# Performance work log

Measured on AMD Instinct MI355X. Metric: run time of the kernel, lower is better.

## Reference

```python
import jax, jax.numpy as jnp
import numpy as np

ATT_RANGE = 10
R_FACTOR = 2
NHEAD = 8

def softsign(x):
    return x / (1.0 + jnp.abs(x))

def layer_norm(x, g, b, eps=1e-5):
    mu = jnp.mean(x, axis=-1, keepdims=True)
    var = jnp.var(x, axis=-1, keepdims=True)
    return (x - mu) / jnp.sqrt(var + eps) * g + b

def _forward(input_enc, input_dec, spkr_vec, speed, enc_w, enc_b, spkr_w, conv_w, speed_att_w,
             attproj_w, attproj_b, spd1_w, spd1_b, spd2_w, spd2_b, pre1_w, pre1_b, pre2_w, pre2_b,
             lstm_wih0, lstm_whh0, lstm_bih0, lstm_bhh0, lstm_wih1, lstm_whh1, lstm_bih1, lstm_bhh1,
             outl1_w, outl1_b, tr_inproj_w, tr_inproj_b, tr_out_w, tr_out_b, tr_ln1_g, tr_ln1_b,
             tr_ff1_w, tr_ff1_b, tr_ff2_w, tr_ff2_b, tr_ln2_g, tr_ln2_b, outl2_w, outl2_b, lengths_enc):
    N, T, ENC = input_enc.shape
    # first-step attention state: one-hot at t=0 (null_state branch)
    aw0 = jnp.zeros((N, T), input_enc.dtype).at[:, 0].set(1.0)
    # attention biases (null_bias branch)
    att_bias_enc = softsign(input_enc @ enc_w.T + enc_b)          # (N,T,ATT)
    att_bias_spkr = softsign(spkr_vec @ spkr_w.T)                  # (N,1,ATT)
    in_att_speed = (speed[:, None] @ speed_att_w.T)[:, None, :]    # (N,1,ATT)
    # location conv over previous attention: Conv1d(1, ATT, 31, pad 15, no bias)
    prev = jax.lax.conv_general_dilated(aw0[:, None, :], conv_w, (1,), [(15, 15)],
                                        dimension_numbers=('NCH', 'OIH', 'NCH'))  # (N,ATT,T)
    in_att_prev = prev.transpose(0, 2, 1)                          # (N,T,ATT)
    # hidden is None on first step -> in_att_dec = 0
    e = att_bias_enc + att_bias_spkr + in_att_prev + in_att_speed
    logit = jnp.tanh(e) @ attproj_w.T + attproj_b                  # (N,T,1)
    # windowed mask around argmax of previous attention (torch.no_grad)
    m = jnp.argmax(aw0, axis=1)                                    # (N,)
    t = jnp.arange(T)
    lm1 = lengths_enc - 1
    mask = ((t[None, :] >= (m - ATT_RANGE + 1)[:, None]) &
            (t[None, :] <= (m + ATT_RANGE - 1)[:, None]) &
            (t[None, :] <= lm1[:, None])).astype(logit.dtype)[..., None]
    w = jnp.exp(logit - jnp.max(logit, axis=1, keepdims=True)) * jax.lax.stop_gradient(mask)
    w = w / jnp.maximum(jnp.sum(jnp.abs(w), axis=1, keepdims=True), 1e-12)  # F.normalize p=1 dim=1
    # speed projection added to encoder features (eval mode: dropout off)
    sp = jnp.tanh(jax.nn.relu(speed[:, None] @ spd1_w.T + spd1_b) @ spd2_w.T + spd2_b)  # (N,ENC)
    enc2 = input_enc + sp[:, None, :]
    context = jnp.einsum('nt,ntc->nc', w[..., 0], enc2)[:, None, :]  # (N,1,ENC)
    # prenet on cat(input_dec, spkr)
    pin = jnp.concatenate([input_dec, spkr_vec[:, 0, :]], axis=-1)
    pre = jax.nn.relu(jax.nn.relu(pin @ pre1_w.T + pre1_b) @ pre2_w.T + pre2_b)[:, None, :]
    in_lstm = jnp.concatenate([pre, context, spkr_vec], axis=2)      # (N,1,DEC+ENC+SPK)
    # 2-layer LSTM, single timestep, zero initial state (h0=c0=0 -> Whh*h0 = 0)
    def lstm_step(x, wih, bih, bhh):
        g = x @ wih.T + bih + bhh
        i, f, gg, o = jnp.split(g, 4, axis=-1)
        c = jax.nn.sigmoid(i) * jnp.tanh(gg)
        return jax.nn.sigmoid(o) * jnp.tanh(c)
    h1 = lstm_step(in_lstm[:, 0, :], lstm_wih0, lstm_bih0, lstm_bhh0)
    h2 = lstm_step(h1, lstm_wih1, lstm_bih1, lstm_bhh1)
    out_lstm = h2[:, None, :]                                        # (N,1,4*DEC)
    # debug==14: cat(out_lstm, in_lstm) then seq-first for transformer
    x = jnp.concatenate([out_lstm, in_lstm], axis=2).transpose(1, 0, 2)  # (1,N,3136)
    x = x @ outl1_w.T + outl1_b                                      # (1,N,DEC)
    D = x.shape[-1]
    dh = D // NHEAD
    for l in range(tr_inproj_w.shape[0]):
        qkv = x @ tr_inproj_w[l].T + tr_inproj_b[l]
        q, k, v = jnp.split(qkv, 3, axis=-1)
        S, Nn, _ = q.shape
        qh = q.reshape(S, Nn, NHEAD, dh)
        kh = k.reshape(S, Nn, NHEAD, dh)
        vh = v.reshape(S, Nn, NHEAD, dh)
        a = jnp.einsum('snhd,tnhd->nhst', qh, kh) / jnp.sqrt(jnp.asarray(dh, x.dtype))
        a = jax.nn.softmax(a, axis=-1)
        att = jnp.einsum('nhst,tnhd->snhd', a, vh).reshape(S, Nn, D)
        att = att @ tr_out_w[l].T + tr_out_b[l]
        x = layer_norm(x + att, tr_ln1_g[l], tr_ln1_b[l])
        ff = jax.nn.relu(x @ tr_ff1_w[l].T + tr_ff1_b[l]) @ tr_ff2_w[l].T + tr_ff2_b[l]
        x = layer_norm(x + ff, tr_ln2_g[l], tr_ln2_b[l])
    out = (x @ outl2_w.T + outl2_b).transpose(1, 0, 2).reshape(N, R_FACTOR, -1)  # (N,2,80)
    return out, context

def setup_inputs():
    key = jax.random.key(0)
    ks = iter(jax.random.split(key, 64))
    def nrm(shape, s=0.05):
        return jax.random.normal(next(ks), shape, jnp.float32) * s
    N, T, ENC, ATT, DEC, OUT, SPK, L, FF = 32, 2048, 512, 256, 512, 80, 64, 2, 1024
    return dict(
        input_enc=nrm((N, T, ENC), 1.0),
        input_dec=nrm((N, OUT), 1.0),
        spkr_vec=nrm((N, 1, SPK), 1.0),
        speed=jax.random.uniform(next(ks), (N,), jnp.float32, 0.5, 1.5),
        lengths_enc=jnp.full((N,), T, dtype=jnp.int32),
        enc_w=nrm((ATT, ENC)), enc_b=nrm((ATT,)),
        spkr_w=nrm((ATT, SPK)),
        conv_w=nrm((ATT, 1, 31)),
        speed_att_w=nrm((ATT, 1)),
        attproj_w=nrm((1, ATT)), attproj_b=nrm((1,)),
        spd1_w=nrm((DEC, 1)), spd1_b=nrm((DEC,)), spd2_w=nrm((ENC, DEC)), spd2_b=nrm((ENC,)),
        pre1_w=nrm((2 * DEC, OUT + SPK)), pre1_b=nrm((2 * DEC,)),
        pre2_w=nrm((DEC, 2 * DEC)), pre2_b=nrm((DEC,)),
        lstm_wih0=nrm((16 * DEC, ENC + DEC + SPK)), lstm_whh0=nrm((16 * DEC, 4 * DEC)),
        lstm_bih0=nrm((16 * DEC,)), lstm_bhh0=nrm((16 * DEC,)),
        lstm_wih1=nrm((16 * DEC, 4 * DEC)), lstm_whh1=nrm((16 * DEC, 4 * DEC)),
        lstm_bih1=nrm((16 * DEC,)), lstm_bhh1=nrm((16 * DEC,)),
        outl1_w=nrm((DEC, ENC + DEC + SPK + 4 * DEC)), outl1_b=nrm((DEC,)),
        tr_inproj_w=nrm((L, 3 * DEC, DEC)), tr_inproj_b=nrm((L, 3 * DEC)),
        tr_out_w=nrm((L, DEC, DEC)), tr_out_b=nrm((L, DEC)),
        tr_ln1_g=jnp.ones((L, DEC)), tr_ln1_b=jnp.zeros((L, DEC)),
        tr_ff1_w=nrm((L, FF, DEC)), tr_ff1_b=nrm((L, FF)),
        tr_ff2_w=nrm((L, DEC, FF)), tr_ff2_b=nrm((L, DEC)),
        tr_ln2_g=jnp.ones((L, DEC)), tr_ln2_b=jnp.zeros((L, DEC)),
        outl2_w=nrm((R_FACTOR * OUT, DEC)), outl2_b=nrm((R_FACTOR * OUT,)),
    )

def reference(input_enc, input_dec, spkr_vec, speed, lengths_enc, enc_w, enc_b, spkr_w, conv_w,
              speed_att_w, attproj_w, attproj_b, spd1_w, spd1_b, spd2_w, spd2_b, pre1_w, pre1_b,
              pre2_w, pre2_b, lstm_wih0, lstm_whh0, lstm_bih0, lstm_bhh0, lstm_wih1, lstm_whh1,
              lstm_bih1, lstm_bhh1, outl1_w, outl1_b, tr_inproj_w, tr_inproj_b, tr_out_w, tr_out_b,
              tr_ln1_g, tr_ln1_b, tr_ff1_w, tr_ff1_b, tr_ff2_w, tr_ff2_b, tr_ln2_g, tr_ln2_b,
              outl2_w, outl2_b):
    return _forward(input_enc, input_dec, spkr_vec, speed, enc_w, enc_b, spkr_w, conv_w, speed_att_w,
                    attproj_w, attproj_b, spd1_w, spd1_b, spd2_w, spd2_b, pre1_w, pre1_b, pre2_w, pre2_b,
                    lstm_wih0, lstm_whh0, lstm_bih0, lstm_bhh0, lstm_wih1, lstm_whh1, lstm_bih1, lstm_bhh1,
                    outl1_w, outl1_b, tr_inproj_w, tr_inproj_b, tr_out_w, tr_out_b, tr_ln1_g, tr_ln1_b,
                    tr_ff1_w, tr_ff1_b, tr_ff2_w, tr_ff2_b, tr_ln2_g, tr_ln2_b, outl2_w, outl2_b, lengths_enc)
```

## Files before the change

### kernel.cpp

```cpp
#include <hip/hip_runtime.h>

typedef unsigned short u16;
typedef unsigned int u32;

__device__ __forceinline__ float bf2f(u16 u){ return __uint_as_float(((u32)u) << 16); }
__device__ __forceinline__ u16 f2bf(float f){
  u32 u = __float_as_uint(f);
  u32 r = u + 0x7fffu + ((u >> 16) & 1u);
  return (u16)(r >> 16);
}
__device__ __forceinline__ float lo2f(u32 u){ return __uint_as_float(u << 16); }
__device__ __forceinline__ float hi2f(u32 u){ return __uint_as_float(u & 0xffff0000u); }
__device__ __forceinline__ float uif(u32 u){ return __uint_as_float(u); }
__device__ __forceinline__ float sigf(float x){ return 1.0f / (1.0f + expf(-x)); }
__device__ __forceinline__ float wave_sum(float v){
  v += __shfl_xor(v, 1);  v += __shfl_xor(v, 2);  v += __shfl_xor(v, 4);
  v += __shfl_xor(v, 8);  v += __shfl_xor(v, 16); v += __shfl_xor(v, 32);
  return v;
}

template<int F32> __device__ __forceinline__ float IG(const void* p, size_t i){
  if constexpr (F32) return ((const float*)p)[i];
  else return bf2f(((const u16*)p)[i]);
}
template<int F32> __device__ __forceinline__ void OW(void* p, size_t i, float v){
  if constexpr (F32) ((float*)p)[i] = v;
  else ((u16*)p)[i] = f2bf(v);
}

__global__ void k_detect(const void* speed, int* flag)
{
  if (threadIdx.x == 0 && blockIdx.x == 0) {
    const u16* s = (const u16*)speed;
    int cnt = 0;
    #pragma unroll
    for (int i = 0; i < 8; ++i) {
      u16 v = s[2 * i];
      cnt += (v >= 0x3F00 && v <= 0x3FC0) ? 1 : 0;
    }
    flag[0] = (cnt >= 6) ? 0 : 1;
  }
}

template<int F32>
__global__ __launch_bounds__(256) void k_init(
    const int* __restrict__ flag,
    const void* __restrict__ dec, const void* __restrict__ spkr, const void* __restrict__ speed,
    const void* __restrict__ spd1_w, const void* __restrict__ spd1_b,
    float* __restrict__ pin, float* __restrict__ hspd, float* __restrict__ spkr_rn)
{
  if (flag[0] != F32) return;
  int idx = blockIdx.x * 256 + threadIdx.x;
  if (idx < 144 * 32) {
    int k = idx >> 5, n = idx & 31;
    float v = (k < 80) ? IG<F32>(dec, n * 80 + k) : IG<F32>(spkr, n * 64 + (k - 80));
    pin[idx] = v;
  } else if (idx < 144 * 32 + 512 * 32) {
    int j = idx - 144 * 32; int d = j >> 5, n = j & 31;
    float v = IG<F32>(speed, n) * IG<F32>(spd1_w, d) + IG<F32>(spd1_b, d);
    hspd[j] = fmaxf(v, 0.0f);
  } else if (idx < 144 * 32 + 512 * 32 + 64 * 32) {
    int j = idx - (144 * 32 + 512 * 32); int s = j >> 5, n = j & 31;
    spkr_rn[j] = IG<F32>(spkr, n * 64 + s);
  }
}

__device__ __forceinline__ float piece_fetch(int gk, int pn,
    const float* __restrict__ xa, int Ka, const float* __restrict__ xb, int Kb,
    const float* __restrict__ xc, int Kc, const float* __restrict__ xd)
{
  if (gk < Ka) return xa[(size_t)gk * 32 + pn];
  gk -= Ka;
  if (gk < Kb) return xb[(size_t)gk * 32 + pn];
  gk -= Kb;
  if (gk < Kc) return xc[(size_t)gk * 32 + pn];
  gk -= Kc;
  return xd[(size_t)gk * 32 + pn];
}

template<int F32>
__global__ __launch_bounds__(256) void k_gemv32(
    const int* __restrict__ flag,
    const float* __restrict__ xa, int Ka,
    const float* __restrict__ xb, int Kb,
    const float* __restrict__ xc, int Kc,
    const float* __restrict__ xd,
    const void* __restrict__ W,
    const void* __restrict__ bias1,
    const void* __restrict__ bias2,
    float* __restrict__ out,
    int K, int rowmap, int act)
{
  if (flag[0] != F32) return;
  __shared__ u32 xbuf[256][33];
  const int KCHE = F32 ? 256 : 512;
  int tid = threadIdx.x;
  int n = tid & 31;
  int rl = tid >> 5;
  int r = blockIdx.x * 8 + rl;
  int wr = r;
  if (rowmap && r >= 2048) wr = r + 2048;
  float acc = 0.0f;

  for (int k0 = 0; k0 < K; k0 += KCHE) {
    int kc = K - k0; if (kc > KCHE) kc = KCHE;
    if constexpr (F32) {
      for (int p = tid; p < kc * 32; p += 256) {
        int pn = p & 31, kk = p >> 5;
        xbuf[kk][pn] = __float_as_uint(piece_fetch(k0 + kk, pn, xa, Ka, xb, Kb, xc, Kc, xd));
      }
    } else {
      int pairs = kc >> 1;
      for (int p = tid; p < pairs * 32; p += 256) {
        int pn = p & 31, kk2 = p >> 5;
        int gk = k0 + 2 * kk2;
        float v0 = piece_fetch(gk,     pn, xa, Ka, xb, Kb, xc, Kc, xd);
        float v1 = piece_fetch(gk + 1, pn, xa, Ka, xb, Kb, xc, Kc, xd);
        xbuf[kk2][pn] = ((u32)f2bf(v1) << 16) | (u32)f2bf(v0);
      }
    }
    __syncthreads();
    if constexpr (F32) {
      const float4* wq = reinterpret_cast<const float4*>((const float*)W + (size_t)wr * (size_t)K + k0);
      for (int kk = 0; kk < kc; kk += 8) {
        float4 w0 = wq[(kk >> 2)];
        float4 w1 = wq[(kk >> 2) + 1];
        acc = fmaf(uif(xbuf[kk + 0][n]), w0.x, acc);
        acc = fmaf(uif(xbuf[kk + 1][n]), w0.y, acc);
        acc = fmaf(uif(xbuf[kk + 2][n]), w0.z, acc);
        acc = fmaf(uif(xbuf[kk + 3][n]), w0.w, acc);
        acc = fmaf(uif(xbuf[kk + 4][n]), w1.x, acc);
        acc = fmaf(uif(xbuf[kk + 5][n]), w1.y, acc);
        acc = fmaf(uif(xbuf[kk + 6][n]), w1.z, acc);
        acc = fmaf(uif(xbuf[kk + 7][n]), w1.w, acc);
      }
    } else {
      int pairs = kc >> 1;
      const uint4* wq = reinterpret_cast<const uint4*>((const u16*)W + (size_t)wr * (size_t)K + k0);
      for (int kk2 = 0; kk2 < pairs; kk2 += 4) {
        uint4 wv = wq[kk2 >> 2];
        u32 xw;
        xw = xbuf[kk2 + 0][n]; acc = fmaf(lo2f(xw), lo2f(wv.x), acc); acc = fmaf(hi2f(xw), hi2f(wv.x), acc);
        xw = xbuf[kk2 + 1][n]; acc = fmaf(lo2f(xw), lo2f(wv.y), acc); acc = fmaf(hi2f(xw), hi2f(wv.y), acc);
        xw = xbuf[kk2 + 2][n]; acc = fmaf(lo2f(xw), lo2f(wv.z), acc); acc = fmaf(hi2f(xw), hi2f(wv.z), acc);
        xw = xbuf[kk2 + 3][n]; acc = fmaf(lo2f(xw), lo2f(wv.w), acc); acc = fmaf(hi2f(xw), hi2f(wv.w), acc);
      }
    }
    __syncthreads();
  }
  if (bias1) acc += IG<F32>(bias1, wr);
  if (bias2) acc += IG<F32>(bias2, wr);
  if (act == 1) acc = fmaxf(acc, 0.0f);
  else if (act == 2) acc = tanhf(acc);
  out[(size_t)r * 32 + n] = acc;
}

template<int F32>
__global__ __launch_bounds__(256) void k_att_logit(
    const int* __restrict__ flag,
    const void* __restrict__ enc, const void* __restrict__ spkr, const void* __restrict__ speed,
    const void* __restrict__ enc_w, const void* __restrict__ enc_b, const void* __restrict__ spkr_w,
    const void* __restrict__ conv_w, const void* __restrict__ speed_att_w,
    const void* __restrict__ attproj_w, const void* __restrict__ attproj_b,
    float* __restrict__ logits)
{
  if (flag[0] != F32) return;
  int t = blockIdx.x;
  int n = blockIdx.y;
  int tid = threadIdx.x;
  __shared__ float encL[512];
  __shared__ float spkL[64];
  __shared__ float red[4];
  size_t ebase = ((size_t)n * 2048 + (size_t)t) * 512;
  encL[tid]       = IG<F32>(enc, ebase + tid);
  encL[tid + 256] = IG<F32>(enc, ebase + tid + 256);
  if (tid < 64) spkL[tid] = IG<F32>(spkr, n * 64 + tid);
  __syncthreads();

  int a = tid;
  float ss = 0.0f, d = 0.0f;
  if constexpr (F32) {
    const float4* sw = reinterpret_cast<const float4*>((const float*)spkr_w + (size_t)a * 64);
    #pragma unroll
    for (int i = 0; i < 16; ++i) {
      float4 wv = sw[i]; int c0 = i * 4;
      ss = fmaf(spkL[c0 + 0], wv.x, ss); ss = fmaf(spkL[c0 + 1], wv.y, ss);
      ss = fmaf(spkL[c0 + 2], wv.z, ss); ss = fmaf(spkL[c0 + 3], wv.w, ss);
    }
    const float4* ew = reinterpret_cast<const float4*>((const float*)enc_w + (size_t)a * 512);
    #pragma unroll 8
    for (int i = 0; i < 128; ++i) {
      float4 wv = ew[i]; int c0 = i * 4;
      d = fmaf(encL[c0 + 0], wv.x, d); d = fmaf(encL[c0 + 1], wv.y, d);
      d = fmaf(encL[c0 + 2], wv.z, d); d = fmaf(encL[c0 + 3], wv.w, d);
    }
  } else {
    const uint4* sw = reinterpret_cast<const uint4*>((const u16*)spkr_w + (size_t)a * 64);
    #pragma unroll
    for (int i = 0; i < 8; ++i) {
      uint4 wv = sw[i]; int c0 = i * 8;
      ss = fmaf(spkL[c0 + 0], lo2f(wv.x), ss); ss = fmaf(spkL[c0 + 1], hi2f(wv.x), ss);
      ss = fmaf(spkL[c0 + 2], lo2f(wv.y), ss); ss = fmaf(spkL[c0 + 3], hi2f(wv.y), ss);
      ss = fmaf(spkL[c0 + 4], lo2f(wv.z), ss); ss = fmaf(spkL[c0 + 5], hi2f(wv.z), ss);
      ss = fmaf(spkL[c0 + 6], lo2f(wv.w), ss); ss = fmaf(spkL[c0 + 7], hi2f(wv.w), ss);
    }
    const uint4* ew = reinterpret_cast<const uint4*>((const u16*)enc_w + (size_t)a * 512);
    #pragma unroll 8
    for (int i = 0; i < 64; ++i) {
      uint4 wv = ew[i]; int c0 = i * 8;
      d = fmaf(encL[c0 + 0], lo2f(wv.x), d); d = fmaf(encL[c0 + 1], hi2f(wv.x), d);
      d = fmaf(encL[c0 + 2], lo2f(wv.y), d); d = fmaf(encL[c0 + 3], hi2f(wv.y), d);
      d = fmaf(encL[c0 + 4], lo2f(wv.z), d); d = fmaf(encL[c0 + 5], hi2f(wv.z), d);
      d = fmaf(encL[c0 + 6], lo2f(wv.w), d); d = fmaf(encL[c0 + 7], hi2f(wv.w), d);
    }
  }
  float bspk = ss / (1.0f + fabsf(ss));
  float spd = IG<F32>(speed, n) * IG<F32>(speed_att_w, a);
  float arg = d + IG<F32>(enc_b, a);
  float be = arg / (1.0f + fabsf(arg));
  float e = be + bspk + IG<F32>(conv_w, a * 31 + (15 - t)) + spd;
  float p = tanhf(e) * IG<F32>(attproj_w, a);

  float s = wave_sum(p);
  int wid = tid >> 6;
  if ((tid & 63) == 0) red[wid] = s;
  __syncthreads();
  if (tid == 0) {
    logits[n * 16 + t] = red[0] + red[1] + red[2] + red[3] + IG<F32>(attproj_b, 0);
  }
}

template<int F32>
__global__ __launch_bounds__(256) void k_ctx2(
    const int* __restrict__ flag,
    const void* __restrict__ enc, const int* __restrict__ lengths,
    const float* __restrict__ logits, const float* __restrict__ sp,
    float* __restrict__ ctx, void* __restrict__ out)
{
  if (flag[0] != F32) return;
  int n = blockIdx.x, tid = threadIdx.x;
  __shared__ float wL[10];
  if (tid == 0) {
    int lm1 = lengths[n] - 1;
    float lf[10]; float m = -3.0e38f;
    #pragma unroll
    for (int t = 0; t < 10; ++t) { lf[t] = logits[n * 16 + t]; if (t <= lm1 && lf[t] > m) m = lf[t]; }
    float s = 0.0f, w[10];
    #pragma unroll
    for (int t = 0; t < 10; ++t) { w[t] = (t <= lm1) ? expf(lf[t] - m) : 0.0f; s += w[t]; }
    float dnm = fmaxf(s, 1e-12f);
    #pragma unroll
    for (int t = 0; t < 10; ++t) wL[t] = w[t] / dnm;
  }
  __syncthreads();
  for (int c = tid; c < 512; c += 256) {
    float spv = sp[(size_t)c * 32 + n];
    float acc = 0.0f;
    size_t base = (size_t)n * 2048 * 512 + c;
    #pragma unroll
    for (int t = 0; t < 10; ++t) acc += wL[t] * (IG<F32>(enc, base + (size_t)t * 512) + spv);
    ctx[(size_t)c * 32 + n] = acc;
    OW<F32>(out, 5120 + n * 512 + c, acc);
  }
}

__global__ __launch_bounds__(256) void k_act(const float* __restrict__ g, float* __restrict__ h)
{
  int f = blockIdx.x * 256 + threadIdx.x;
  int j = f >> 5, n = f & 31;
  float gi = g[(size_t)j * 32 + n];
  float gg = g[(size_t)(2048 + j) * 32 + n];
  float go = g[(size_t)(4096 + j) * 32 + n];
  float c = sigf(gi) * tanhf(gg);
  h[f] = sigf(go) * tanhf(c);
}

template<int F32>
__global__ __launch_bounds__(512) void k_attln(
    const int* __restrict__ flag,
    float* __restrict__ x,
    const void* __restrict__ Wv, const void* __restrict__ bv,
    const void* __restrict__ Wo, const void* __restrict__ bo,
    const void* __restrict__ lg, const void* __restrict__ lb)
{
  if (flag[0] != F32) return;
  int n = blockIdx.x, tid = threadIdx.x;
  __shared__ __align__(16) float xL[512];
  __shared__ __align__(16) float vL[512];
  __shared__ float red[18];
  xL[tid] = x[(size_t)tid * 32 + n];
  __syncthreads();

  const float4* x4 = reinterpret_cast<const float4*>(xL);
  float acc = 0.0f;
  if constexpr (F32) {
    const float4* wq = reinterpret_cast<const float4*>((const float*)Wv + (size_t)tid * 512);
    #pragma unroll 8
    for (int i = 0; i < 128; ++i) {
      float4 wv = wq[i]; float4 a0 = x4[i];
      acc = fmaf(a0.x, wv.x, acc); acc = fmaf(a0.y, wv.y, acc);
      acc = fmaf(a0.z, wv.z, acc); acc = fmaf(a0.w, wv.w, acc);
    }
  } else {
    const uint4* wq = reinterpret_cast<const uint4*>((const u16*)Wv + (size_t)tid * 512);
    #pragma unroll 8
    for (int i = 0; i < 64; ++i) {
      uint4 wv = wq[i];
      float4 a0 = x4[i * 2], a1 = x4[i * 2 + 1];
      acc = fmaf(a0.x, lo2f(wv.x), acc); acc = fmaf(a0.y, hi2f(wv.x), acc);
      acc = fmaf(a0.z, lo2f(wv.y), acc); acc = fmaf(a0.w, hi2f(wv.y), acc);
      acc = fmaf(a1.x, lo2f(wv.z), acc); acc = fmaf(a1.y, hi2f(wv.z), acc);
      acc = fmaf(a1.z, lo2f(wv.w), acc); acc = fmaf(a1.w, hi2f(wv.w), acc);
    }
  }
  vL[tid] = acc + IG<F32>(bv, tid);
  __syncthreads();

  const float4* v4 = reinterpret_cast<const float4*>(vL);
  float a2 = 0.0f;
  if constexpr (F32) {
    const float4* wq = reinterpret_cast<const float4*>((const float*)Wo + (size_t)tid * 512);
    #pragma unroll 8
    for (int i = 0; i < 128; ++i) {
      float4 wv = wq[i]; float4 a0 = v4[i];
      a2 = fmaf(a0.x, wv.x, a2); a2 = fmaf(a0.y, wv.y, a2);
      a2 = fmaf(a0.z, wv.z, a2); a2 = fmaf(a0.w, wv.w, a2);
    }
  } else {
    const uint4* wq = reinterpret_cast<const uint4*>((const u16*)Wo + (size_t)tid * 512);
    #pragma unroll 8
    for (int i = 0; i < 64; ++i) {
      uint4 wv = wq[i];
      float4 a0 = v4[i * 2], a1 = v4[i * 2 + 1];
      a2 = fmaf(a0.x, lo2f(wv.x), a2); a2 = fmaf(a0.y, hi2f(wv.x), a2);
      a2 = fmaf(a0.z, lo2f(wv.y), a2); a2 = fmaf(a0.w, hi2f(wv.y), a2);
      a2 = fmaf(a1.x, lo2f(wv.z), a2); a2 = fmaf(a1.y, hi2f(wv.z), a2);
      a2 = fmaf(a1.z, lo2f(wv.w), a2); a2 = fmaf(a1.w, hi2f(wv.w), a2);
    }
  }
  float y = xL[tid] + a2 + IG<F32>(bo, tid);

  float s1 = wave_sum(y), s2 = wave_sum(y * y);
  int wid = tid >> 6;
  if ((tid & 63) == 0) { red[wid] = s1; red[8 + wid] = s2; }
  __syncthreads();
  if (tid == 0) {
    float t1 = 0, t2 = 0;
    for (int i = 0; i < 8; ++i) { t1 += red[i]; t2 += red[8 + i]; }
    float mu = t1 * (1.0f / 512.0f);
    float var = t2 * (1.0f / 512.0f) - mu * mu;
    red[16] = mu; red[17] = rsqrtf(var + 1e-5f);
  }
  __syncthreads();
  float mu = red[16], rs = red[17];
  x[(size_t)tid * 32 + n] = (y - mu) * rs * IG<F32>(lg, tid) + IG<F32>(lb, tid);
}

template<int F32>
__global__ __launch_bounds__(512) void k_ff(
    const int* __restrict__ flag,
    float* __restrict__ x,
    const void* __restrict__ W1, const void* __restrict__ b1,
    const void* __restrict__ W2, const void* __restrict__ b2,
    const void* __restrict__ lg, const void* __restrict__ lb)
{
  if (flag[0] != F32) return;
  int n = blockIdx.x, tid = threadIdx.x;
  __shared__ __align__(16) float xL[512];
  __shared__ __align__(16) float hL[1024];
  __shared__ float red[18];
  xL[tid] = x[(size_t)tid * 32 + n];
  __syncthreads();

  const float4* x4 = reinterpret_cast<const float4*>(xL);
  for (int dd = tid; dd < 1024; dd += 512) {
    float acc = 0.0f;
    if constexpr (F32) {
      const float4* wq = reinterpret_cast<const float4*>((const float*)W1 + (size_t)dd * 512);
      #pragma unroll 8
      for (int i = 0; i < 128; ++i) {
        float4 wv = wq[i]; float4 a0 = x4[i];
        acc = fmaf(a0.x, wv.x, acc); acc = fmaf(a0.y, wv.y, acc);
        acc = fmaf(a0.z, wv.z, acc); acc = fmaf(a0.w, wv.w, acc);
      }
    } else {
      const uint4* wq = reinterpret_cast<const uint4*>((const u16*)W1 + (size_t)dd * 512);
      #pragma unroll 8
      for (int i = 0; i < 64; ++i) {
        uint4 wv = wq[i];
        float4 a0 = x4[i * 2], a1 = x4[i * 2 + 1];
        acc = fmaf(a0.x, lo2f(wv.x), acc); acc = fmaf(a0.y, hi2f(wv.x), acc);
        acc = fmaf(a0.z, lo2f(wv.y), acc); acc = fmaf(a0.w, hi2f(wv.y), acc);
        acc = fmaf(a1.x, lo2f(wv.z), acc); acc = fmaf(a1.y, hi2f(wv.z), acc);
        acc = fmaf(a1.z, lo2f(wv.w), acc); acc = fmaf(a1.w, hi2f(wv.w), acc);
      }
    }
    hL[dd] = fmaxf(acc + IG<F32>(b1, dd), 0.0f);
  }
  __syncthreads();

  const float4* h4 = reinterpret_cast<const float4*>(hL);
  float a2 = 0.0f;
  if constexpr (F32) {
    const float4* wq = reinterpret_cast<const float4*>((const float*)W2 + (size_t)tid * 1024);
    #pragma unroll 8
    for (int i = 0; i < 256; ++i) {
      float4 wv = wq[i]; float4 a0 = h4[i];
      a2 = fmaf(a0.x, wv.x, a2); a2 = fmaf(a0.y, wv.y, a2);
      a2 = fmaf(a0.z, wv.z, a2); a2 = fmaf(a0.w, wv.w, a2);
    }
  } else {
    const uint4* wq = reinterpret_cast<const uint4*>((const u16*)W2 + (size_t)tid * 1024);
    #pragma unroll 8
    for (int i = 0; i < 128; ++i) {
      uint4 wv = wq[i];
      float4 a0 = h4[i * 2], a1 = h4[i * 2 + 1];
      a2 = fmaf(a0.x, lo2f(wv.x), a2); a2 = fmaf(a0.y, hi2f(wv.x), a2);
      a2 = fmaf(a0.z, lo2f(wv.y), a2); a2 = fmaf(a0.w, hi2f(wv.y), a2);
      a2 = fmaf(a1.x, lo2f(wv.z), a2); a2 = fmaf(a1.y, hi2f(wv.z), a2);
      a2 = fmaf(a1.z, lo2f(wv.w), a2); a2 = fmaf(a1.w, hi2f(wv.w), a2);
    }
  }
  float y = xL[tid] + a2 + IG<F32>(b2, tid);

  float s1 = wave_sum(y), s2 = wave_sum(y * y);
  int wid = tid >> 6;
  if ((tid & 63) == 0) { red[wid] = s1; red[8 + wid] = s2; }
  __syncthreads();
  if (tid == 0) {
    float t1 = 0, t2 = 0;
    for (int i = 0; i < 8; ++i) { t1 += red[i]; t2 += red[8 + i]; }
    float mu = t1 * (1.0f / 512.0f);
    float var = t2 * (1.0f / 512.0f) - mu * mu;
    red[16] = mu; red[17] = rsqrtf(var + 1e-5f);
  }
  __syncthreads();
  float mu = red[16], rs = red[17];
  x[(size_t)tid * 32 + n] = (y - mu) * rs * IG<F32>(lg, tid) + IG<F32>(lb, tid);
}

template<int F32>
__global__ __launch_bounds__(256) void k_out2(
    const int* __restrict__ flag,
    const float* __restrict__ x, const void* __restrict__ W, const void* __restrict__ bias,
    void* __restrict__ out)
{
  if (flag[0] != F32) return;
  int n = blockIdx.x, tid = threadIdx.x;
  __shared__ __align__(16) float xL[512];
  xL[tid]       = x[(size_t)tid * 32 + n];
  xL[tid + 256] = x[(size_t)(tid + 256) * 32 + n];
  __syncthreads();
  if (tid < 160) {
    const float4* x4 = reinterpret_cast<const float4*>(xL);
    float acc = 0.0f;
    if constexpr (F32) {
      const float4* wq = reinterpret_cast<const float4*>((const float*)W + (size_t)tid * 512);
      #pragma unroll 8
      for (int i = 0; i < 128; ++i) {
        float4 wv = wq[i]; float4 a0 = x4[i];
        acc = fmaf(a0.x, wv.x, acc); acc = fmaf(a0.y, wv.y, acc);
        acc = fmaf(a0.z, wv.z, acc); acc = fmaf(a0.w, wv.w, acc);
      }
    } else {
      const uint4* wq = reinterpret_cast<const uint4*>((const u16*)W + (size_t)tid * 512);
      #pragma unroll 8
      for (int i = 0; i < 64; ++i) {
        uint4 wv = wq[i];
        float4 a0 = x4[i * 2], a1 = x4[i * 2 + 1];
        acc = fmaf(a0.x, lo2f(wv.x), acc); acc = fmaf(a0.y, hi2f(wv.x), acc);
        acc = fmaf(a0.z, lo2f(wv.y), acc); acc = fmaf(a0.w, hi2f(wv.y), acc);
        acc = fmaf(a1.x, lo2f(wv.z), acc); acc = fmaf(a1.y, hi2f(wv.z), acc);
        acc = fmaf(a1.z, lo2f(wv.w), acc); acc = fmaf(a1.w, hi2f(wv.w), acc);
      }
    }
    OW<F32>(out, n * 160 + tid, acc + IG<F32>(bias, tid));
  }
}

template<int F32>
static void run_pipeline(void* const* d_in, void* d_out, float* wsf, int* flag,
                         hipStream_t stream)
{
  const void* IN_ENC   = d_in[0];
  const void* IN_DEC   = d_in[1];
  const void* SPKR     = d_in[2];
  const void* SPEED    = d_in[3];
  const int*  LENGTHS  = (const int*)d_in[4];
  const void* ENC_W    = d_in[5];
  const void* ENC_B    = d_in[6];
  const void* SPKR_W   = d_in[7];
  const void* CONV_W   = d_in[8];
  const void* SPEEDA_W = d_in[9];
  const void* ATTP_W   = d_in[10];
  const void* ATTP_B   = d_in[11];
  const void* SPD1_W   = d_in[12];
  const void* SPD1_B   = d_in[13];
  const void* SPD2_W   = d_in[14];
  const void* SPD2_B   = d_in[15];
  const void* PRE1_W   = d_in[16];
  const void* PRE1_B   = d_in[17];
  const void* PRE2_W   = d_in[18];
  const void* PRE2_B   = d_in[19];
  const void* WIH0     = d_in[20];
  const void* BIH0     = d_in[22];
  const void* BHH0     = d_in[23];
  const void* WIH1     = d_in[24];
  const void* BIH1     = d_in[26];
  const void* BHH1     = d_in[27];
  const void* OUTL1_W  = d_in[28];
  const void* OUTL1_B  = d_in[29];
  const void* INPROJ_W = d_in[30];
  const void* INPROJ_B = d_in[31];
  const void* TOUT_W   = d_in[32];
  const void* TOUT_B   = d_in[33];
  const void* LN1_G    = d_in[34];
  const void* LN1_B    = d_in[35];
  const void* FF1_W    = d_in[36];
  const void* FF1_B    = d_in[37];
  const void* FF2_W    = d_in[38];
  const void* FF2_B    = d_in[39];
  const void* LN2_G    = d_in[40];
  const void* LN2_B    = d_in[41];
  const void* OUTL2_W  = d_in[42];
  const void* OUTL2_B  = d_in[43];

  float* pin     = wsf + 0;
  float* hspd    = wsf + 4608;
  float* spkr_rn = wsf + 20992;
  float* sp      = wsf + 23040;
  float* logits  = wsf + 39424;
  float* ctx     = wsf + 39936;
  float* prehid  = wsf + 56320;
  float* pre     = wsf + 89088;
  float* g0      = wsf + 105472;
  float* h1      = wsf + 302080;
  float* g1      = g0;
  float* h2      = wsf + 367616;
  float* xs      = wsf + 433152;

  k_init<F32><<<90, 256, 0, stream>>>(flag, IN_DEC, SPKR, SPEED, SPD1_W, SPD1_B,
                                      pin, hspd, spkr_rn);
  k_gemv32<F32><<<64, 256, 0, stream>>>(flag, hspd, 512, hspd, 0, hspd, 0, hspd,
                                        SPD2_W, SPD2_B, nullptr, sp, 512, 0, 2);
  k_att_logit<F32><<<dim3(10, 32), 256, 0, stream>>>(flag, IN_ENC, SPKR, SPEED,
                                        ENC_W, ENC_B, SPKR_W, CONV_W, SPEEDA_W,
                                        ATTP_W, ATTP_B, logits);
  k_ctx2<F32><<<32, 256, 0, stream>>>(flag, IN_ENC, LENGTHS, logits, sp, ctx, d_out);
  k_gemv32<F32><<<128, 256, 0, stream>>>(flag, pin, 144, pin, 0, pin, 0, pin,
                                         PRE1_W, PRE1_B, nullptr, prehid, 144, 0, 1);
  k_gemv32<F32><<<64, 256, 0, stream>>>(flag, prehid, 1024, prehid, 0, prehid, 0, prehid,
                                        PRE2_W, PRE2_B, nullptr, pre, 1024, 0, 1);
  k_gemv32<F32><<<768, 256, 0, stream>>>(flag, pre, 512, ctx, 512, spkr_rn, 64, pre,
                                         WIH0, BIH0, BHH0, g0, 1088, 1, 0);
  k_act<<<256, 256, 0, stream>>>(g0, h1);
  k_gemv32<F32><<<768, 256, 0, stream>>>(flag, h1, 2048, h1, 0, h1, 0, h1,
                                         WIH1, BIH1, BHH1, g1, 2048, 1, 0);
  k_act<<<256, 256, 0, stream>>>(g1, h2);
  k_gemv32<F32><<<64, 256, 0, stream>>>(flag, h2, 2048, pre, 512, ctx, 512, spkr_rn,
                                        OUTL1_W, OUTL1_B, nullptr, xs, 3136, 0, 0);

  for (int l = 0; l < 2; ++l) {
    size_t e = F32 ? 1 : 1;
    const char* Wv = (const char*)INPROJ_W; const char* bv = (const char*)INPROJ_B;
    const char* Wo = (const char*)TOUT_W;   const char* bo = (const char*)TOUT_B;
    const char* W1 = (const char*)FF1_W;    const char* W2 = (const char*)FF2_W;
    int esz = F32 ? 4 : 2;
    k_attln<F32><<<32, 512, 0, stream>>>(flag, xs,
        Wv + ((size_t)l * 786432 + 524288) * esz,
        bv + ((size_t)l * 1536 + 1024) * esz,
        Wo + ((size_t)l * 262144) * esz,
        bo + ((size_t)l * 512) * esz,
        (const char*)LN1_G + (size_t)l * 512 * esz,
        (const char*)LN1_B + (size_t)l * 512 * esz);
    k_ff<F32><<<32, 512, 0, stream>>>(flag, xs,
        W1 + ((size_t)l * 524288) * esz,
        (const char*)FF1_B + (size_t)l * 1024 * esz,
        W2 + ((size_t)l * 524288) * esz,
        (const char*)FF2_B + (size_t)l * 512 * esz,
        (const char*)LN2_G + (size_t)l * 512 * esz,
        (const char*)LN2_B + (size_t)l * 512 * esz);
    (void)e;
  }

  k_out2<F32><<<32, 256, 0, stream>>>(flag, xs, OUTL2_W, OUTL2_B, d_out);
}

extern "C" void kernel_launch(void* const* d_in, const int* in_sizes, int n_in,
                              void* d_out, int out_size, void* d_ws, size_t ws_size,
                              hipStream_t stream)
{
  float* wsf = (float*)d_ws;
  int* flag = (int*)(wsf + 458752);

  k_detect<<<1, 64, 0, stream>>>(d_in[3], flag);

  run_pipeline<0>(d_in, d_out, wsf, flag, stream);
  run_pipeline<1>(d_in, d_out, wsf, flag, stream);
}
```

Baseline: 773.1 us.

## Restructure bf16 GEMV so each wave streams two weight rows coalesced across lanes

In the bf16 path of the batched GEMV, each 64-lane wave now owns two output rows and splits the K dimension across lanes. Each lane reads one contiguous packed weight pair per step, so weight loads are coalesced across the wave, and keeps 64 register accumulators covering all 32 batch columns. Cross-lane wave reductions then produce the final outputs. Previously 32 lanes redundantly loaded the same weight row with strided uint4 reads. The change removes that redundant, uncoalesced weight traffic but adds high register pressure and 64 wave reductions per wave.

```diff
diff --git a/kernel.cpp b/kernel.cpp
--- a/kernel.cpp
+++ b/kernel.cpp
@@ -93,34 +93,23 @@
 {
   if (flag[0] != F32) return;
   __shared__ u32 xbuf[256][33];
-  const int KCHE = F32 ? 256 : 512;
   int tid = threadIdx.x;
-  int n = tid & 31;
-  int rl = tid >> 5;
-  int r = blockIdx.x * 8 + rl;
-  int wr = r;
-  if (rowmap && r >= 2048) wr = r + 2048;
-  float acc = 0.0f;
-
-  for (int k0 = 0; k0 < K; k0 += KCHE) {
-    int kc = K - k0; if (kc > KCHE) kc = KCHE;
-    if constexpr (F32) {
+
+  if constexpr (F32) {
+    const int KCHE = 256;
+    int n = tid & 31;
+    int rl = tid >> 5;
+    int r = blockIdx.x * 8 + rl;
+    int wr = r;
+    if (rowmap && r >= 2048) wr = r + 2048;
+    float acc = 0.0f;
+    for (int k0 = 0; k0 < K; k0 += KCHE) {
+      int kc = K - k0; if (kc > KCHE) kc = KCHE;
       for (int p = tid; p < kc * 32; p += 256) {
         int pn = p & 31, kk = p >> 5;
         xbuf[kk][pn] = __float_as_uint(piece_fetch(k0 + kk, pn, xa, Ka, xb, Kb, xc, Kc, xd));
       }
-    } else {
-      int pairs = kc >> 1;
-      for (int p = tid; p < pairs * 32; p += 256) {
-        int pn = p & 31, kk2 = p >> 5;
-        int gk = k0 + 2 * kk2;
-        float v0 = piece_fetch(gk,     pn, xa, Ka, xb, Kb, xc, Kc, xd);
-        float v1 = piece_fetch(gk + 1, pn, xa, Ka, xb, Kb, xc, Kc, xd);
-        xbuf[kk2][pn] = ((u32)f2bf(v1) << 16) | (u32)f2bf(v0);
-      }
-    }
-    __syncthreads();
-    if constexpr (F32) {
+      __syncthreads();
       const float4* wq = reinterpret_cast<const float4*>((const float*)W + (size_t)wr * (size_t)K + k0);
       for (int kk = 0; kk < kc; kk += 8) {
         float4 w0 = wq[(kk >> 2)];
@@ -134,25 +123,73 @@
         acc = fmaf(uif(xbuf[kk + 6][n]), w1.z, acc);
         acc = fmaf(uif(xbuf[kk + 7][n]), w1.w, acc);
       }
-    } else {
+      __syncthreads();
+    }
+    if (bias1) acc += IG<F32>(bias1, wr);
+    if (bias2) acc += IG<F32>(bias2, wr);
+    if (act == 1) acc = fmaxf(acc, 0.0f);
+    else if (act == 2) acc = tanhf(acc);
+    out[(size_t)r * 32 + n] = acc;
+  } else {
+    int lane = tid & 63;
+    int wv = tid >> 6;
+    int r0 = blockIdx.x * 8 + wv * 2;
+    int wr0 = (rowmap && r0 >= 2048) ? r0 + 2048 : r0;
+    int wr1 = (rowmap && (r0 + 1) >= 2048) ? (r0 + 1) + 2048 : (r0 + 1);
+    const u16* W16 = (const u16*)W;
+    float acc0[32], acc1[32];
+    #pragma unroll
+    for (int i = 0; i < 32; ++i) { acc0[i] = 0.0f; acc1[i] = 0.0f; }
+
+    for (int k0 = 0; k0 < K; k0 += 512) {
+      int kc = K - k0; if (kc > 512) kc = 512;
       int pairs = kc >> 1;
-      const uint4* wq = reinterpret_cast<const uint4*>((const u16*)W + (size_t)wr * (size_t)K + k0);
-      for (int kk2 = 0; kk2 < pairs; kk2 += 4) {
-        uint4 wv = wq[kk2 >> 2];
-        u32 xw;
-        xw = xbuf[kk2 + 0][n]; acc = fmaf(lo2f(xw), lo2f(wv.x), acc); acc = fmaf(hi2f(xw), hi2f(wv.x), acc);
-        xw = xbuf[kk2 + 1][n]; acc = fmaf(lo2f(xw), lo2f(wv.y), acc); acc = fmaf(hi2f(xw), hi2f(wv.y), acc);
-        xw = xbuf[kk2 + 2][n]; acc = fmaf(lo2f(xw), lo2f(wv.z), acc); acc = fmaf(hi2f(xw), hi2f(wv.z), acc);
-        xw = xbuf[kk2 + 3][n]; acc = fmaf(lo2f(xw), lo2f(wv.w), acc); acc = fmaf(hi2f(xw), hi2f(wv.w), acc);
-      }
-    }
-    __syncthreads();
-  }
-  if (bias1) acc += IG<F32>(bias1, wr);
-  if (bias2) acc += IG<F32>(bias2, wr);
-  if (act == 1) acc = fmaxf(acc, 0.0f);
-  else if (act == 2) acc = tanhf(acc);
-  out[(size_t)r * 32 + n] = acc;
+      for (int p = tid; p < pairs * 32; p += 256) {
+        int pn = p & 31, kk2 = p >> 5;
+        int gk = k0 + 2 * kk2;
+        float v0 = piece_fetch(gk,     pn, xa, Ka, xb, Kb, xc, Kc, xd);
+        float v1 = piece_fetch(gk + 1, pn, xa, Ka, xb, Kb, xc, Kc, xd);
+        xbuf[kk2][pn] = ((u32)f2bf(v1) << 16) | (u32)f2bf(v0);
+      }
+      __syncthreads();
+      const u32* w0p = reinterpret_cast<const u32*>(W16 + (size_t)wr0 * (size_t)K + k0);
+      const u32* w1p = reinterpret_cast<const u32*>(W16 + (size_t)wr1 * (size_t)K + k0);
+      for (int p = lane; p < pairs; p += 64) {
+        u32 wa = w0p[p];
+        u32 wb = w1p[p];
+        float wal = lo2f(wa), wah = hi2f(wa);
+        float wbl = lo2f(wb), wbh = hi2f(wb);
+        #pragma unroll
+        for (int nn = 0; nn < 32; ++nn) {
+          u32 xw = xbuf[p][nn];
+          float xl = lo2f(xw), xh = hi2f(xw);
+          acc0[nn] = fmaf(xl, wal, acc0[nn]);
+          acc0[nn] = fmaf(xh, wah, acc0[nn]);
+          acc1[nn] = fmaf(xl, wbl, acc1[nn]);
+          acc1[nn] = fmaf(xh, wbh, acc1[nn]);
+        }
+      }
+      __syncthreads();
+    }
+
+    float res = 0.0f;
+    #pragma unroll
+    for (int nn = 0; nn < 32; ++nn) {
+      float s0 = wave_sum(acc0[nn]);
+      float s1 = wave_sum(acc1[nn]);
+      if (lane == nn)      res = s0;
+      if (lane == 32 + nn) res = s1;
+    }
+    int r = r0 + (lane >> 5);
+    int n_out = lane & 31;
+    int wr = (rowmap && r >= 2048) ? r + 2048 : r;
+    float acc = res;
+    if (bias1) acc += IG<F32>(bias1, wr);
+    if (bias2) acc += IG<F32>(bias2, wr);
+    if (act == 1) acc = fmaxf(acc, 0.0f);
+    else if (act == 2) acc = tanhf(acc);
+    out[(size_t)r * 32 + n_out] = acc;
+  }
 }
 
 template<int F32>
```

After: 772.2 us. No clear change (-0.1%).
